# Optimization experiments

Measured on AMD Instinct MI355X. Metric: run time of the kernel, lower is better.

## Reference

```python
import jax, jax.numpy as jnp
import numpy as np

ALPHA = 0.2  # LeakyReLU negative slope (undefined global `alpha` in source; canonical GAT value)
MASK_VAL = -9e15


def setup_inputs() -> dict:
    key = jax.random.key(0)
    k = jax.random.split(key, 6)
    B, N, D = 8, 2048, 256
    x = jax.random.normal(k[0], (B, N, D), dtype=jnp.float32)
    adj = jax.random.randint(k[1], (B, N, N), 0, 2, dtype=jnp.int32)
    W = jax.random.normal(k[2], (D, D), dtype=jnp.float32) * (1.414 / np.sqrt(D))
    a = jax.random.normal(k[3], (2 * D, 1), dtype=jnp.float32) * 0.1
    han_w = jax.random.normal(k[4], (D, D), dtype=jnp.float32) / np.sqrt(D)
    han_b = jax.random.normal(k[5], (D,), dtype=jnp.float32) * 0.01
    return {"x": x, "adj": adj, "W": W, "a": a, "han_w": han_w, "han_b": han_b}


def reference(x, adj, W, a, han_w, han_b):
    B, N, D = x.shape
    h = jnp.matmul(x, W)                              # [B,N,D]
    a1 = jnp.matmul(x, a[:D])                         # [B,N,1]
    a2 = jnp.matmul(x, a[D:])                         # [B,N,1]
    # e[b,i,j] = leakyrelu(a1[b,i] + a2[b,j])
    e = jax.nn.leaky_relu(a1 + jnp.swapaxes(a2, 1, 2), negative_slope=ALPHA)  # [B,N,N]
    att = jnp.where(adj > 0, e, MASK_VAL)
    # NOTE: source softmaxes over dim=1 (source-node axis), faithfully reproduced
    att = jax.nn.softmax(att, axis=1)
    h_prime = jnp.matmul(att, h)                      # [B,N,D]
    hid = jax.nn.elu(h_prime)                         # concat=True branch
    return jnp.matmul(hid, han_w) + han_b
```

## Files before the change

kernel.cpp:

```cpp
#include <hip/hip_runtime.h>
#include <hip/hip_bf16.h>
#include <stdint.h>

#define B_ 8
#define N_ 2048
#define D_ 256
#define BN (B_*N_)
#define NSEG 64
#define SROWS 32

typedef __bf16 bf16;
typedef bf16 bf16x8 __attribute__((ext_vector_type(8)));
typedef bf16 bf16x4 __attribute__((ext_vector_type(4)));
typedef float f32x4 __attribute__((ext_vector_type(4)));

__device__ __forceinline__ void gload16(const void* g, void* l) {
  __builtin_amdgcn_global_load_lds(
      (const __attribute__((address_space(1))) unsigned int*)g,
      (__attribute__((address_space(3))) unsigned int*)l,
      16, 0, 0);
}

__global__ __launch_bounds__(256) void k_transpose_w(
    const float* __restrict__ w, const float* __restrict__ hw,
    bf16* __restrict__ wt, bf16* __restrict__ hwt) {
  int t = blockIdx.x * 256 + threadIdx.x;
  int d = t >> 8, k = t & 255;
  wt[t]  = (bf16)w[k * D_ + d];
  hwt[t] = (bf16)hw[k * D_ + d];
}

__global__ __launch_bounds__(256) void k_gemm_h(
    const float* __restrict__ x, const bf16* __restrict__ wt,
    const float* __restrict__ avec, bf16* __restrict__ hT,
    float* __restrict__ a1, float* __restrict__ e1, float* __restrict__ f1,
    float* __restrict__ a2, float* __restrict__ e2, float* __restrict__ f2) {
  int blk = blockIdx.x;
  int b = blk >> 5;
  int j0 = (blk & 31) * 64;
  int w = threadIdx.x >> 6, l = threadIdx.x & 63;
  int jr = j0 + w * 16 + (l & 15);
  const float* xrow = x + ((size_t)(b * N_ + jr)) * D_;
  int koff = 8 * (l >> 4);
  f32x4 acc[16];
  #pragma unroll
  for (int i = 0; i < 16; ++i) acc[i] = f32x4{0.f, 0.f, 0.f, 0.f};
  float s1 = 0.f, s2 = 0.f;
  for (int kb = 0; kb < D_; kb += 32) {
    float4 xa = *(const float4*)(xrow + kb + koff);
    float4 xb = *(const float4*)(xrow + kb + koff + 4);
    float4 ua = *(const float4*)(avec + kb + koff);
    float4 ub = *(const float4*)(avec + kb + koff + 4);
    float4 va = *(const float4*)(avec + D_ + kb + koff);
    float4 vb = *(const float4*)(avec + D_ + kb + koff + 4);
    s1 = fmaf(xa.x, ua.x, fmaf(xa.y, ua.y, fmaf(xa.z, ua.z, fmaf(xa.w, ua.w, s1))));
    s1 = fmaf(xb.x, ub.x, fmaf(xb.y, ub.y, fmaf(xb.z, ub.z, fmaf(xb.w, ub.w, s1))));
    s2 = fmaf(xa.x, va.x, fmaf(xa.y, va.y, fmaf(xa.z, va.z, fmaf(xa.w, va.w, s2))));
    s2 = fmaf(xb.x, vb.x, fmaf(xb.y, vb.y, fmaf(xb.z, vb.z, fmaf(xb.w, vb.w, s2))));
    bf16x8 af = { (bf16)xa.x, (bf16)xa.y, (bf16)xa.z, (bf16)xa.w,
                  (bf16)xb.x, (bf16)xb.y, (bf16)xb.z, (bf16)xb.w };
    #pragma unroll
    for (int dt = 0; dt < 16; ++dt) {
      bf16x8 bfr = *(const bf16x8*)(wt + (dt * 16 + (l & 15)) * D_ + kb + koff);
      acc[dt] = __builtin_amdgcn_mfma_f32_16x16x32_bf16(af, bfr, acc[dt], 0, 0, 0);
    }
  }
  s1 += __shfl_xor(s1, 16); s1 += __shfl_xor(s1, 32);
  s2 += __shfl_xor(s2, 16); s2 += __shfl_xor(s2, 32);
  if (l < 16) {
    int row = b * N_ + j0 + w * 16 + l;
    a1[row] = s1; e1[row] = __expf(s1); f1[row] = __expf(0.2f * s1);
    a2[row] = s2; e2[row] = __expf(s2); f2[row] = __expf(0.2f * s2);
  }
  int jw = j0 + w * 16 + (l >> 4) * 4;
  #pragma unroll
  for (int dt = 0; dt < 16; ++dt) {
    int d = dt * 16 + (l & 15);
    bf16x4 o = { (bf16)acc[dt][0], (bf16)acc[dt][1], (bf16)acc[dt][2], (bf16)acc[dt][3] };
    *(bf16x4*)(hT + ((size_t)(b * D_ + d)) * N_ + jw) = o;
  }
}

__global__ __launch_bounds__(512) void k_colstats(
    const int* __restrict__ adj,
    const float* __restrict__ a1, const float* __restrict__ e1, const float* __restrict__ f1,
    const float* __restrict__ a2,
    float* __restrict__ partA, float* __restrict__ partB,
    unsigned char* __restrict__ maskB) {
  int blk = blockIdx.x;
  int b  = blk >> 6;
  int is = blk & (NSEG - 1);
  int t = threadIdx.x;
  int grp = t >> 8, tt = t & 255;
  int ibase = is * SROWS + grp * 16;
  __shared__ float a1s[SROWS], e1s[SROWS], f1s[SROWS];
  __shared__ float redA[256 * 8], redB[256 * 8];
  if (t < SROWS) {
    int gi = b * N_ + is * SROWS + t;
    a1s[t] = a1[gi]; e1s[t] = e1[gi]; f1s[t] = f1[gi];
  }
  __syncthreads();
  int j0 = tt * 8;
  float4 a2lo = *(const float4*)(a2 + b * N_ + j0);
  float4 a2hi = *(const float4*)(a2 + b * N_ + j0 + 4);
  float a2v[8] = {a2lo.x, a2lo.y, a2lo.z, a2lo.w, a2hi.x, a2hi.y, a2hi.z, a2hi.w};
  float SA[8], SB[8];
  #pragma unroll
  for (int e = 0; e < 8; ++e) { SA[e] = 0.f; SB[e] = 0.f; }
  const int* arow = adj + ((size_t)(b * N_ + ibase)) * N_ + j0;
  unsigned char* mrow = maskB + (size_t)(b * N_ + ibase) * (N_ / 8) + tt;
  #pragma unroll 4
  for (int ii = 0; ii < 16; ++ii) {
    int4 v0 = *(const int4*)(arow + (size_t)ii * N_);
    int4 v1 = *(const int4*)(arow + (size_t)ii * N_ + 4);
    int sr = grp * 16 + ii;
    float a1i = a1s[sr], e1i = e1s[sr], f1i = f1s[sr];
    int vals[8] = {v0.x, v0.y, v0.z, v0.w, v1.x, v1.y, v1.z, v1.w};
    unsigned int mb = 0;
    #pragma unroll
    for (int e = 0; e < 8; ++e) {
      bool pred = vals[e] != 0;
      mb |= pred ? (1u << e) : 0u;
      float ttv = a1i + a2v[e];
      bool gt = ttv > 0.f;
      SA[e] += (pred && gt)  ? e1i : 0.f;
      SB[e] += (pred && !gt) ? f1i : 0.f;
    }
    mrow[(size_t)ii * (N_ / 8)] = (unsigned char)mb;
  }
  if (grp == 1) {
    #pragma unroll
    for (int e = 0; e < 8; ++e) { redA[tt * 8 + e] = SA[e]; redB[tt * 8 + e] = SB[e]; }
  }
  __syncthreads();
  if (grp == 0) {
    #pragma unroll
    for (int e = 0; e < 8; ++e) { SA[e] += redA[tt * 8 + e]; SB[e] += redB[tt * 8 + e]; }
    float* pA = partA + ((size_t)(b * NSEG + is)) * N_ + j0;
    float* pB = partB + ((size_t)(b * NSEG + is)) * N_ + j0;
    *(float4*)(pA)     = float4{SA[0], SA[1], SA[2], SA[3]};
    *(float4*)(pA + 4) = float4{SA[4], SA[5], SA[6], SA[7]};
    *(float4*)(pB)     = float4{SB[0], SB[1], SB[2], SB[3]};
    *(float4*)(pB + 4) = float4{SB[4], SB[5], SB[6], SB[7]};
  }
}

__global__ __launch_bounds__(256) void k_colfin(
    const float* __restrict__ partA, const float* __restrict__ partB,
    const float* __restrict__ e2, const float* __restrict__ f2,
    float* __restrict__ e2rs, float* __restrict__ f2rs) {
  int g = blockIdx.x * 256 + threadIdx.x;
  int b = g >> 11, j = g & (N_ - 1);
  float SA = 0.f, SB = 0.f;
  #pragma unroll 8
  for (int is = 0; is < NSEG; ++is) {
    SA += partA[((size_t)(b * NSEG + is)) * N_ + j];
    SB += partB[((size_t)(b * NSEG + is)) * N_ + j];
  }
  float s = e2[g] * SA + f2[g] * SB;
  float rs = s > 0.f ? 1.f / s : 0.f;
  e2rs[g] = e2[g] * rs;
  f2rs[g] = f2[g] * rs;
}

__global__ __launch_bounds__(512, 2) void k_attmm(
    const bf16* __restrict__ hT, const unsigned char* __restrict__ maskB,
    const float* __restrict__ a1v, const float* __restrict__ e1v, const float* __restrict__ f1v,
    const float* __restrict__ a2v, const float* __restrict__ e2rs, const float* __restrict__ f2rs,
    const bf16* __restrict__ hwt, const float* __restrict__ hb,
    float* __restrict__ out) {
  __shared__ __attribute__((aligned(128))) char smem[120 * 1024];
  char* s_b = smem;
  char* s_a = smem + 65536;
  float* s_src = (float*)(smem + 81920);
  unsigned char* s_mask = (unsigned char*)(smem + 106496);
  char* s_hid = smem;
  char* s_mrg = smem + 32768;

  int blk = blockIdx.x;
  int b  = blk & 7;
  int i0 = (blk >> 3) * 64;
  int t = threadIdx.x, w = t >> 6, l = t & 63;
  int l15 = l & 15, lg = l >> 4;
  int dwm = w & 3, kh = w >> 2;

  #pragma unroll
  for (int s = 0; s < 3; ++s) {
    int idx = t + s * 512;
    int arr = idx >> 9, pos = (idx & 511) * 4;
    const float* src = (arr == 0) ? (a2v + b * N_) : (arr == 1) ? (e2rs + b * N_) : (f2rs + b * N_);
    *(float4*)(s_src + arr * N_ + pos) = *(const float4*)(src + pos);
  }
  {
    int row = t >> 3, seg = t & 7;
    const unsigned long long* g = (const unsigned long long*)
        (maskB + ((size_t)(b * N_ + i0 + row)) * (N_ / 8) + seg * 32);
    int sw = (row & 31) << 3;
    #pragma unroll
    for (int k2 = 0; k2 < 4; ++k2) {
      int cb = seg * 32 + k2 * 8;
      *(unsigned long long*)(s_mask + row * 256 + (cb ^ sw)) = g[k2];
    }
  }

  int ib = t >> 3, jq = t & 7;
  int gi = b * N_ + i0 + ib;
  float a1i = a1v[gi], e1i = e1v[gi], f1i = f1v[gi];
  int mswz = (ib & 31) << 3;
  const unsigned char* mline = s_mask + ib * 256;
  const bf16* hTb = hT + (size_t)b * D_ * N_;

  f32x4 acc[4][4];
  #pragma unroll
  for (int is = 0; is < 4; ++is)
    #pragma unroll
    for (int ds = 0; ds < 4; ++ds) acc[is][ds] = f32x4{0.f, 0.f, 0.f, 0.f};

  __syncthreads();

  #define STAGE_B(KB, NB) do {                                              \
    char* dstb = s_b + (NB) * 32768;                                        \
    _Pragma("unroll")                                                       \
    for (int r = 0; r < 4; ++r) {                                           \
      int c = r * 512 + t;                                                  \
      int dd = c >> 3, sub = c & 7;                                         \
      int ssub = sub ^ (dd & 7);                                            \
      gload16(hTb + (size_t)dd * N_ + (KB) + ssub * 8, dstb + c * 16);      \
    }                                                                       \
  } while (0)

  #define BUILD_A(KB, NB) do {                                              \
    int jb = (KB) + jq * 8;                                                 \
    float4 p0 = *(const float4*)(s_src + jb);                               \
    float4 p1 = *(const float4*)(s_src + jb + 4);                           \
    float4 q0 = *(const float4*)(s_src + N_ + jb);                          \
    float4 q1 = *(const float4*)(s_src + N_ + jb + 4);                      \
    float4 r0 = *(const float4*)(s_src + 2 * N_ + jb);                      \
    float4 r1 = *(const float4*)(s_src + 2 * N_ + jb + 4);                  \
    unsigned int m = mline[((((KB) >> 3) + jq)) ^ mswz];                    \
    float a2x[8] = {p0.x,p0.y,p0.z,p0.w,p1.x,p1.y,p1.z,p1.w};               \
    float evx[8] = {q0.x,q0.y,q0.z,q0.w,q1.x,q1.y,q1.z,q1.w};               \
    float fvx[8] = {r0.x,r0.y,r0.z,r0.w,r1.x,r1.y,r1.z,r1.w};               \
    bf16x8 av;                                                              \
    _Pragma("unroll")                                                       \
    for (int e = 0; e < 8; ++e) {                                           \
      float tt2 = a1i + a2x[e];                                             \
      bool sel = tt2 > 0.f;                                                 \
      float vv = (sel ? e1i : f1i) * (sel ? evx[e] : fvx[e]);               \
      vv = ((m >> e) & 1u) ? vv : 0.f;                                      \
      av[e] = (bf16)vv;                                                     \
    }                                                                       \
    *(bf16x8*)(s_a + (NB) * 8192 + ib * 128 + ((jq ^ (ib & 7)) * 16)) = av; \
  } while (0)

  STAGE_B(0, 0);
  BUILD_A(0, 0);
  __syncthreads();

  int kq = kh * 4 + lg;
  int cur = 0;
  for (int ks = 0; ks < 32; ++ks) {
    if (ks < 31) {
      int kbn = (ks + 1) * 64;
      STAGE_B(kbn, cur ^ 1);
      BUILD_A(kbn, cur ^ 1);
    }
    const char* sa = s_a + cur * 8192;
    const char* sb = s_b + cur * 32768;
    bf16x8 afr[4], bfr[4];
    #pragma unroll
    for (int is = 0; is < 4; ++is) {
      int ra = is * 16 + l15;
      afr[is] = *(const bf16x8*)(sa + ra * 128 + ((kq ^ (ra & 7)) * 16));
    }
    #pragma unroll
    for (int ds = 0; ds < 4; ++ds) {
      int rb = dwm * 64 + ds * 16 + l15;
      bfr[ds] = *(const bf16x8*)(sb + rb * 128 + ((kq ^ (rb & 7)) * 16));
    }
    #pragma unroll
    for (int is = 0; is < 4; ++is)
      #pragma unroll
      for (int ds = 0; ds < 4; ++ds)
        acc[is][ds] = __builtin_amdgcn_mfma_f32_16x16x32_bf16(
            afr[is], bfr[ds], acc[is][ds], 0, 0, 0);
    __syncthreads();
    cur ^= 1;
  }

  if (kh == 1) {
    #pragma unroll
    for (int is = 0; is < 4; ++is)
      #pragma unroll
      for (int ds = 0; ds < 4; ++ds)
        *(f32x4*)(s_mrg + (size_t)dwm * 16384 + ((is * 4 + ds) * 64 + l) * 16) = acc[is][ds];
  }
  __syncthreads();
  if (kh == 0) {
    #pragma unroll
    for (int is = 0; is < 4; ++is) {
      #pragma unroll
      for (int ds = 0; ds < 4; ++ds) {
        f32x4 o = *(const f32x4*)(s_mrg + (size_t)dwm * 16384 + ((is * 4 + ds) * 64 + l) * 16);
        f32x4 sm = acc[is][ds] + o;
        int d = dwm * 64 + ds * 16 + l15;
        int c = d >> 3, dby = (d & 7) * 2;
        #pragma unroll
        for (int r = 0; r < 4; ++r) {
          int il = is * 16 + lg * 4 + r;
          float vv = sm[r];
          float hv = vv > 0.f ? vv : __expf(vv) - 1.f;
          *(bf16*)(s_hid + il * 512 + ((c ^ (il & 31)) * 16) + dby) = (bf16)hv;
        }
      }
    }
  }
  __syncthreads();

  int iw2 = w & 1, dw2 = w >> 1;
  f32x4 acc2[2][4];
  #pragma unroll
  for (int is = 0; is < 2; ++is)
    #pragma unroll
    for (int ds = 0; ds < 4; ++ds) acc2[is][ds] = f32x4{0.f, 0.f, 0.f, 0.f};
  #pragma unroll
  for (int kh2 = 0; kh2 < 8; ++kh2) {
    int kc = kh2 * 4 + lg;
    bf16x8 afr2[2];
    #pragma unroll
    for (int is = 0; is < 2; ++is) {
      int ra = iw2 * 32 + is * 16 + l15;
      afr2[is] = *(const bf16x8*)(s_hid + ra * 512 + ((kc ^ (ra & 31)) * 16));
    }
    #pragma unroll
    for (int ds = 0; ds < 4; ++ds) {
      int d2 = dw2 * 64 + ds * 16 + l15;
      bf16x8 bfr2 = *(const bf16x8*)(hwt + (size_t)d2 * D_ + kh2 * 32 + lg * 8);
      #pragma unroll
      for (int is = 0; is < 2; ++is)
        acc2[is][ds] = __builtin_amdgcn_mfma_f32_16x16x32_bf16(
            afr2[is], bfr2, acc2[is][ds], 0, 0, 0);
    }
  }
  #pragma unroll
  for (int is = 0; is < 2; ++is) {
    #pragma unroll
    for (int ds = 0; ds < 4; ++ds) {
      int d = dw2 * 64 + ds * 16 + l15;
      float bias = hb[d];
      #pragma unroll
      for (int r = 0; r < 4; ++r) {
        int i = i0 + iw2 * 32 + is * 16 + lg * 4 + r;
        out[((size_t)(b * N_ + i)) * D_ + d] = acc2[is][ds][r] + bias;
      }
    }
  }
}

extern "C" void kernel_launch(void* const* d_in, const int* in_sizes, int n_in,
                              void* d_out, int out_size, void* d_ws, size_t ws_size,
                              hipStream_t stream) {
  (void)in_sizes; (void)n_in; (void)out_size; (void)ws_size;
  const float* x   = (const float*)d_in[0];
  const int*   adj = (const int*)d_in[1];
  const float* W   = (const float*)d_in[2];
  const float* a   = (const float*)d_in[3];
  const float* hw  = (const float*)d_in[4];
  const float* hb  = (const float*)d_in[5];
  float* out = (float*)d_out;

  char* ws = (char*)d_ws;
  size_t off = 0;
  auto alloc = [&](size_t bytes) -> char* {
    char* p = ws + off;
    off += (bytes + 255) & ~(size_t)255;
    return p;
  };
  float* a1   = (float*)alloc(BN * 4);
  float* e1   = (float*)alloc(BN * 4);
  float* f1   = (float*)alloc(BN * 4);
  float* a2   = (float*)alloc(BN * 4);
  float* e2   = (float*)alloc(BN * 4);
  float* f2   = (float*)alloc(BN * 4);
  float* e2rs = (float*)alloc(BN * 4);
  float* f2rs = (float*)alloc(BN * 4);
  float* partA = (float*)alloc((size_t)B_ * NSEG * N_ * 4);
  float* partB = (float*)alloc((size_t)B_ * NSEG * N_ * 4);
  unsigned char* maskB = (unsigned char*)alloc((size_t)BN * (N_ / 8));
  bf16* hT  = (bf16*)alloc((size_t)B_ * D_ * N_ * 2);
  bf16* wt  = (bf16*)alloc((size_t)D_ * D_ * 2);
  bf16* hwt = (bf16*)alloc((size_t)D_ * D_ * 2);

  k_transpose_w<<<256, 256, 0, stream>>>(W, hw, wt, hwt);
  k_gemm_h<<<256, 256, 0, stream>>>(x, wt, a, hT, a1, e1, f1, a2, e2, f2);
  k_colstats<<<B_ * NSEG, 512, 0, stream>>>(adj, a1, e1, f1, a2, partA, partB, maskB);
  k_colfin<<<BN / 256, 256, 0, stream>>>(partA, partB, e2, f2, e2rs, f2rs);
  k_attmm<<<256, 512, 0, stream>>>(hT, maskB, a1, e1, f1, a2, e2rs, f2rs,
                                   hwt, hb, out);
}
```

Baseline: 112.0 us.

## Halve attmm row tile to 32 rows, drop K-split, double grid

The attention-matmul kernel now processes 32 rows per block instead of 64 and launches 512 blocks instead of 256, so the grid covers more of the GPU's compute units. The split-K across wave halves and its LDS merge step are removed. The a2/e2rs/f2rs vectors and mask bits are no longer staged in shared memory and are read straight from global memory. Shared memory per block drops to 72KB and launch bounds allow more blocks per CU. The trade-off is that each block re-streams the full hT B-operand for half as many rows, which doubles global and L2 traffic for hT, and MFMA work per B-tile load is lower.

```diff
diff --git a/kernel.cpp b/kernel.cpp
--- a/kernel.cpp
+++ b/kernel.cpp
@@ -163,60 +163,36 @@
   f2rs[g] = f2[g] * rs;
 }
 
-__global__ __launch_bounds__(512, 2) void k_attmm(
+__global__ __launch_bounds__(512, 4) void k_attmm(
     const bf16* __restrict__ hT, const unsigned char* __restrict__ maskB,
     const float* __restrict__ a1v, const float* __restrict__ e1v, const float* __restrict__ f1v,
     const float* __restrict__ a2v, const float* __restrict__ e2rs, const float* __restrict__ f2rs,
     const bf16* __restrict__ hwt, const float* __restrict__ hb,
     float* __restrict__ out) {
-  __shared__ __attribute__((aligned(128))) char smem[120 * 1024];
+  __shared__ __attribute__((aligned(128))) char smem[72 * 1024];
   char* s_b = smem;
   char* s_a = smem + 65536;
-  float* s_src = (float*)(smem + 81920);
-  unsigned char* s_mask = (unsigned char*)(smem + 106496);
   char* s_hid = smem;
-  char* s_mrg = smem + 32768;
 
   int blk = blockIdx.x;
   int b  = blk & 7;
-  int i0 = (blk >> 3) * 64;
+  int i0 = (blk >> 3) * 32;
   int t = threadIdx.x, w = t >> 6, l = t & 63;
   int l15 = l & 15, lg = l >> 4;
-  int dwm = w & 3, kh = w >> 2;
-
-  #pragma unroll
-  for (int s = 0; s < 3; ++s) {
-    int idx = t + s * 512;
-    int arr = idx >> 9, pos = (idx & 511) * 4;
-    const float* src = (arr == 0) ? (a2v + b * N_) : (arr == 1) ? (e2rs + b * N_) : (f2rs + b * N_);
-    *(float4*)(s_src + arr * N_ + pos) = *(const float4*)(src + pos);
-  }
-  {
-    int row = t >> 3, seg = t & 7;
-    const unsigned long long* g = (const unsigned long long*)
-        (maskB + ((size_t)(b * N_ + i0 + row)) * (N_ / 8) + seg * 32);
-    int sw = (row & 31) << 3;
-    #pragma unroll
-    for (int k2 = 0; k2 < 4; ++k2) {
-      int cb = seg * 32 + k2 * 8;
-      *(unsigned long long*)(s_mask + row * 256 + (cb ^ sw)) = g[k2];
-    }
-  }
-
-  int ib = t >> 3, jq = t & 7;
+  int iw = w & 1, dw = w >> 1;
+
+  int ib = t >> 4, jq = t & 15;
   int gi = b * N_ + i0 + ib;
   float a1i = a1v[gi], e1i = e1v[gi], f1i = f1v[gi];
-  int mswz = (ib & 31) << 3;
-  const unsigned char* mline = s_mask + ib * 256;
+  const unsigned char* mline = maskB + (size_t)gi * (N_ / 8);
+  const float* a2b = a2v + b * N_;
+  const float* eb  = e2rs + b * N_;
+  const float* fb  = f2rs + b * N_;
   const bf16* hTb = hT + (size_t)b * D_ * N_;
 
-  f32x4 acc[4][4];
-  #pragma unroll
-  for (int is = 0; is < 4; ++is)
-    #pragma unroll
-    for (int ds = 0; ds < 4; ++ds) acc[is][ds] = f32x4{0.f, 0.f, 0.f, 0.f};
-
-  __syncthreads();
+  f32x4 acc[4];
+  #pragma unroll
+  for (int ds = 0; ds < 4; ++ds) acc[ds] = f32x4{0.f, 0.f, 0.f, 0.f};
 
   #define STAGE_B(KB, NB) do {                                              \
     char* dstb = s_b + (NB) * 32768;                                        \
@@ -230,34 +206,33 @@
   } while (0)
 
   #define BUILD_A(KB, NB) do {                                              \
-    int jb = (KB) + jq * 8;                                                 \
-    float4 p0 = *(const float4*)(s_src + jb);                               \
-    float4 p1 = *(const float4*)(s_src + jb + 4);                           \
-    float4 q0 = *(const float4*)(s_src + N_ + jb);                          \
-    float4 q1 = *(const float4*)(s_src + N_ + jb + 4);                      \
-    float4 r0 = *(const float4*)(s_src + 2 * N_ + jb);                      \
-    float4 r1 = *(const float4*)(s_src + 2 * N_ + jb + 4);                  \
-    unsigned int m = mline[((((KB) >> 3) + jq)) ^ mswz];                    \
-    float a2x[8] = {p0.x,p0.y,p0.z,p0.w,p1.x,p1.y,p1.z,p1.w};               \
-    float evx[8] = {q0.x,q0.y,q0.z,q0.w,q1.x,q1.y,q1.z,q1.w};               \
-    float fvx[8] = {r0.x,r0.y,r0.z,r0.w,r1.x,r1.y,r1.z,r1.w};               \
-    bf16x8 av;                                                              \
+    int jb = (KB) + jq * 4;                                                 \
+    float4 p = *(const float4*)(a2b + jb);                                  \
+    float4 q = *(const float4*)(eb + jb);                                   \
+    float4 r = *(const float4*)(fb + jb);                                   \
+    unsigned int byte = mline[((KB) >> 3) + (jq >> 1)];                     \
+    unsigned int nib = (byte >> ((jq & 1) * 4)) & 0xFu;                     \
+    float a2x[4] = {p.x, p.y, p.z, p.w};                                    \
+    float evx[4] = {q.x, q.y, q.z, q.w};                                    \
+    float fvx[4] = {r.x, r.y, r.z, r.w};                                    \
+    bf16x4 av;                                                              \
     _Pragma("unroll")                                                       \
-    for (int e = 0; e < 8; ++e) {                                           \
+    for (int e = 0; e < 4; ++e) {                                           \
       float tt2 = a1i + a2x[e];                                             \
       bool sel = tt2 > 0.f;                                                 \
       float vv = (sel ? e1i : f1i) * (sel ? evx[e] : fvx[e]);               \
-      vv = ((m >> e) & 1u) ? vv : 0.f;                                      \
+      vv = ((nib >> e) & 1u) ? vv : 0.f;                                    \
       av[e] = (bf16)vv;                                                     \
     }                                                                       \
-    *(bf16x8*)(s_a + (NB) * 8192 + ib * 128 + ((jq ^ (ib & 7)) * 16)) = av; \
+    int chunk = jq >> 1;                                                    \
+    *(bf16x4*)(s_a + (NB) * 4096 + ib * 128 +                               \
+               ((chunk ^ (ib & 7)) * 16) + (jq & 1) * 8) = av;              \
   } while (0)
 
   STAGE_B(0, 0);
   BUILD_A(0, 0);
   __syncthreads();
 
-  int kq = kh * 4 + lg;
   int cur = 0;
   for (int ks = 0; ks < 32; ++ks) {
     if (ks < 31) {
@@ -265,94 +240,64 @@
       STAGE_B(kbn, cur ^ 1);
       BUILD_A(kbn, cur ^ 1);
     }
-    const char* sa = s_a + cur * 8192;
+    const char* sa = s_a + cur * 4096;
     const char* sb = s_b + cur * 32768;
-    bf16x8 afr[4], bfr[4];
-    #pragma unroll
-    for (int is = 0; is < 4; ++is) {
-      int ra = is * 16 + l15;
-      afr[is] = *(const bf16x8*)(sa + ra * 128 + ((kq ^ (ra & 7)) * 16));
-    }
-    #pragma unroll
-    for (int ds = 0; ds < 4; ++ds) {
-      int rb = dwm * 64 + ds * 16 + l15;
-      bfr[ds] = *(const bf16x8*)(sb + rb * 128 + ((kq ^ (rb & 7)) * 16));
-    }
-    #pragma unroll
-    for (int is = 0; is < 4; ++is)
+    #pragma unroll
+    for (int kh = 0; kh < 2; ++kh) {
+      int kq = kh * 4 + lg;
+      int ra = iw * 16 + l15;
+      bf16x8 afr = *(const bf16x8*)(sa + ra * 128 + ((kq ^ (ra & 7)) * 16));
+      bf16x8 bfr[4];
+      #pragma unroll
+      for (int ds = 0; ds < 4; ++ds) {
+        int rb = dw * 64 + ds * 16 + l15;
+        bfr[ds] = *(const bf16x8*)(sb + rb * 128 + ((kq ^ (rb & 7)) * 16));
+      }
       #pragma unroll
       for (int ds = 0; ds < 4; ++ds)
-        acc[is][ds] = __builtin_amdgcn_mfma_f32_16x16x32_bf16(
-            afr[is], bfr[ds], acc[is][ds], 0, 0, 0);
+        acc[ds] = __builtin_amdgcn_mfma_f32_16x16x32_bf16(afr, bfr[ds], acc[ds], 0, 0, 0);
+    }
     __syncthreads();
     cur ^= 1;
   }
 
-  if (kh == 1) {
-    #pragma unroll
-    for (int is = 0; is < 4; ++is)
-      #pragma unroll
-      for (int ds = 0; ds < 4; ++ds)
-        *(f32x4*)(s_mrg + (size_t)dwm * 16384 + ((is * 4 + ds) * 64 + l) * 16) = acc[is][ds];
+  #pragma unroll
+  for (int ds = 0; ds < 4; ++ds) {
+    int d = dw * 64 + ds * 16 + l15;
+    int c = d >> 3, dby = (d & 7) * 2;
+    #pragma unroll
+    for (int r = 0; r < 4; ++r) {
+      int il = iw * 16 + lg * 4 + r;
+      float vv = acc[ds][r];
+      float hv = vv > 0.f ? vv : __expf(vv) - 1.f;
+      *(bf16*)(s_hid + il * 512 + ((c ^ (il & 31)) * 16) + dby) = (bf16)hv;
+    }
   }
   __syncthreads();
-  if (kh == 0) {
-    #pragma unroll
-    for (int is = 0; is < 4; ++is) {
-      #pragma unroll
-      for (int ds = 0; ds < 4; ++ds) {
-        f32x4 o = *(const f32x4*)(s_mrg + (size_t)dwm * 16384 + ((is * 4 + ds) * 64 + l) * 16);
-        f32x4 sm = acc[is][ds] + o;
-        int d = dwm * 64 + ds * 16 + l15;
-        int c = d >> 3, dby = (d & 7) * 2;
-        #pragma unroll
-        for (int r = 0; r < 4; ++r) {
-          int il = is * 16 + lg * 4 + r;
-          float vv = sm[r];
-          float hv = vv > 0.f ? vv : __expf(vv) - 1.f;
-          *(bf16*)(s_hid + il * 512 + ((c ^ (il & 31)) * 16) + dby) = (bf16)hv;
-        }
-      }
-    }
-  }
-  __syncthreads();
-
-  int iw2 = w & 1, dw2 = w >> 1;
-  f32x4 acc2[2][4];
-  #pragma unroll
-  for (int is = 0; is < 2; ++is)
-    #pragma unroll
-    for (int ds = 0; ds < 4; ++ds) acc2[is][ds] = f32x4{0.f, 0.f, 0.f, 0.f};
+
+  f32x4 acc2[4];
+  #pragma unroll
+  for (int ds = 0; ds < 4; ++ds) acc2[ds] = f32x4{0.f, 0.f, 0.f, 0.f};
   #pragma unroll
   for (int kh2 = 0; kh2 < 8; ++kh2) {
     int kc = kh2 * 4 + lg;
-    bf16x8 afr2[2];
-    #pragma unroll
-    for (int is = 0; is < 2; ++is) {
-      int ra = iw2 * 32 + is * 16 + l15;
-      afr2[is] = *(const bf16x8*)(s_hid + ra * 512 + ((kc ^ (ra & 31)) * 16));
-    }
+    int ra = iw * 16 + l15;
+    bf16x8 afr2 = *(const bf16x8*)(s_hid + ra * 512 + ((kc ^ (ra & 31)) * 16));
     #pragma unroll
     for (int ds = 0; ds < 4; ++ds) {
-      int d2 = dw2 * 64 + ds * 16 + l15;
+      int d2 = dw * 64 + ds * 16 + l15;
       bf16x8 bfr2 = *(const bf16x8*)(hwt + (size_t)d2 * D_ + kh2 * 32 + lg * 8);
-      #pragma unroll
-      for (int is = 0; is < 2; ++is)
-        acc2[is][ds] = __builtin_amdgcn_mfma_f32_16x16x32_bf16(
-            afr2[is], bfr2, acc2[is][ds], 0, 0, 0);
-    }
-  }
-  #pragma unroll
-  for (int is = 0; is < 2; ++is) {
-    #pragma unroll
-    for (int ds = 0; ds < 4; ++ds) {
-      int d = dw2 * 64 + ds * 16 + l15;
-      float bias = hb[d];
-      #pragma unroll
-      for (int r = 0; r < 4; ++r) {
-        int i = i0 + iw2 * 32 + is * 16 + lg * 4 + r;
-        out[((size_t)(b * N_ + i)) * D_ + d] = acc2[is][ds][r] + bias;
-      }
+      acc2[ds] = __builtin_amdgcn_mfma_f32_16x16x32_bf16(afr2, bfr2, acc2[ds], 0, 0, 0);
+    }
+  }
+  #pragma unroll
+  for (int ds = 0; ds < 4; ++ds) {
+    int d = dw * 64 + ds * 16 + l15;
+    float bias = hb[d];
+    #pragma unroll
+    for (int r = 0; r < 4; ++r) {
+      int i = i0 + iw * 16 + lg * 4 + r;
+      out[((size_t)(b * N_ + i)) * D_ + d] = acc2[ds][r] + bias;
     }
   }
 }
@@ -395,6 +340,6 @@
   k_gemm_h<<<256, 256, 0, stream>>>(x, wt, a, hT, a1, e1, f1, a2, e2, f2);
   k_colstats<<<B_ * NSEG, 512, 0, stream>>>(adj, a1, e1, f1, a2, partA, partB, maskB);
   k_colfin<<<BN / 256, 256, 0, stream>>>(partA, partB, e2, f2, e2rs, f2rs);
-  k_attmm<<<256, 512, 0, stream>>>(hT, maskB, a1, e1, f1, a2, e2rs, f2rs,
+  k_attmm<<<512, 512, 0, stream>>>(hT, maskB, a1, e1, f1, a2, e2rs, f2rs,
                                    hwt, hb, out);
 }
```

Result: slower. 115.2 us (+2.9%).
